# Performance work log

Hardware: AMD Instinct MI355X
Metric: run time of the kernel (lower is better)

The kernel has to match this reference:

```python
import jax, jax.numpy as jnp
import numpy as np
from jax import lax

BIG = jnp.float32(1e10)  # initial 'infinite' min-distance


def farthest_point_sampling(points, nsamples):
    """Exact iterative FPS. points: (B, P, 3) -> indices (B, nsamples) int32.

    The KD-tree partitioning in QuickFPS is an acceleration structure; the
    reference math is the canonical running-min-distance / argmax FPS.
    """
    B, P, _ = points.shape

    def step(carry, _):
        min_d, last_idx = carry
        # (B, 1, 3) coordinates of the most recently selected point
        last_pt = jnp.take_along_axis(points, last_idx[:, None, None], axis=1)
        d = jnp.sum((points - last_pt) ** 2, axis=-1)  # (B, P)
        min_d = jnp.minimum(min_d, d)
        nxt = jnp.argmax(min_d, axis=-1).astype(jnp.int32)  # (B,)
        return (min_d, nxt), nxt

    init_idx = jnp.zeros((B,), jnp.int32)  # CUDA FPS starts from point 0
    init_d = jnp.full((B, P), BIG, dtype=points.dtype)
    (_, _), rest = lax.scan(step, (init_d, init_idx), None, length=nsamples - 1)
    # rest: (nsamples-1, B) -> (B, nsamples)
    indices = jnp.concatenate([init_idx[None, :], rest], axis=0).T
    return indices


def setup_inputs() -> dict:
    key = jax.random.key(0)
    points = jax.random.normal(key, (32, 65536, 3), dtype=jnp.float32)
    return {"points": points}


def reference(points):
    nsamples = 1024
    indices = farthest_point_sampling(points, nsamples)  # (B, nsamples)
    # gather_points: (B, nsamples, 3)
    sampled_points = jnp.take_along_axis(points, indices[:, :, None], axis=1)
    return indices, sampled_points
```

## Files before the change

kernel.cpp:

```cpp
#include <hip/hip_runtime.h>

#define NB 32
#define NP 65536
#define NS 1024
#define NT 1024

typedef unsigned long long u64;
typedef unsigned int u32;

#define BPB 8
#define CHUNK (NP / BPB)
#define PPT2 (CHUNK / NT)

__global__ __launch_bounds__(NT) void fps_slots(const float* __restrict__ pts,
                                                float* __restrict__ out,
                                                u64* __restrict__ slots) {
#pragma clang fp contract(off)
    const int bid = blockIdx.x;
    const int b = bid >> 3;
    const int j = bid & 7;
    const int t = threadIdx.x;
    const int base = j * CHUNK;
    const float* __restrict__ pb = pts + (size_t)b * NP * 3;
    float* __restrict__ out_idx = out + (size_t)b * NS;
    float* __restrict__ out_pts = out + (size_t)NB * NS + (size_t)b * NS * 3;
    u64* __restrict__ slot_b = slots + (size_t)b * NS * BPB;

    __shared__ float P[CHUNK * 3];
    __shared__ u64 cand[NT / 64];
    __shared__ int sel_hist[NS];
    __shared__ float qsh[3];

    {
        const float4* __restrict__ src4 = (const float4*)(pb + (size_t)base * 3);
        float4* dst4 = (float4*)P;
#pragma unroll
        for (int k = 0; k < (CHUNK * 3 / 4) / NT; ++k) dst4[t + k * NT] = src4[t + k * NT];
    }

    float md[PPT2];
#pragma unroll
    for (int i = 0; i < PPT2; ++i) md[i] = 1e10f;

    if (t == 0) {
        sel_hist[0] = 0;
        if (j == 0) out_idx[0] = 0.0f;
        qsh[0] = pb[0]; qsh[1] = pb[1]; qsh[2] = pb[2];
    }
    __syncthreads();

    float qx = qsh[0], qy = qsh[1], qz = qsh[2];

    const int wave = t >> 6;
    const int lane = t & 63;

    for (int s = 1; s < NS; ++s) {
        float bestv = -1.0f;
        int besti = 0;
#pragma unroll
        for (int i = 0; i < PPT2; ++i) {
            const int li = t + i * NT;
            const float* __restrict__ p = P + li * 3;
            float dx = p[0] - qx;
            float dy = p[1] - qy;
            float dz = p[2] - qz;
            float d = (dx * dx + dy * dy) + dz * dz;
            float nmd = fminf(md[i], d);
            md[i] = nmd;
            if (nmd > bestv) { bestv = nmd; besti = li; }
        }
        u64 pk = ((u64)__float_as_uint(bestv) << 32) |
                 (u64)(0xFFFFFFFFu - (u32)(base + besti));
#pragma unroll
        for (int m = 32; m >= 1; m >>= 1) {
            u64 o = __shfl_xor(pk, m, 64);
            pk = (o > pk) ? o : pk;
        }
        if (lane == 0) cand[wave] = pk;
        __syncthreads();
        if (wave == 0) {
            u64 c = (lane < 16) ? cand[lane] : 0ull;
#pragma unroll
            for (int m = 8; m >= 1; m >>= 1) {
                u64 o = __shfl_xor(c, m, 64);
                c = (o > c) ? o : c;
            }
            if (lane == 0) {
                __hip_atomic_store(&slot_b[(size_t)s * BPB + j], c,
                                   __ATOMIC_RELAXED, __HIP_MEMORY_SCOPE_AGENT);
            }
            u64 x = 0;
            if (lane < BPB) {
                const u64* sp = &slot_b[(size_t)s * BPB + lane];
                while ((x = __hip_atomic_load(sp, __ATOMIC_RELAXED,
                                              __HIP_MEMORY_SCOPE_AGENT)) == 0ull) {
                    __builtin_amdgcn_s_sleep(1);
                }
            }
#pragma unroll
            for (int m = 4; m >= 1; m >>= 1) {
                u64 o = __shfl_xor(x, m, 64);
                x = (o > x) ? o : x;
            }
            if (lane == 0) {
                int w = (int)(0xFFFFFFFFu - (u32)(x & 0xFFFFFFFFull));
                sel_hist[s] = w;
                const float* __restrict__ q = pb + (size_t)w * 3;
                qsh[0] = q[0]; qsh[1] = q[1]; qsh[2] = q[2];
                if (j == 0) out_idx[s] = (float)w;
            }
        }
        __syncthreads();
        qx = qsh[0]; qy = qsh[1]; qz = qsh[2];
    }

    if (j == 0) {
        const int gi = sel_hist[t];
        const float* __restrict__ p = pb + (size_t)gi * 3;
        out_pts[(size_t)t * 3 + 0] = p[0];
        out_pts[(size_t)t * 3 + 1] = p[1];
        out_pts[(size_t)t * 3 + 2] = p[2];
    }
}

__global__ __launch_bounds__(NT) void fps_multi(const float* __restrict__ pts,
                                                float* __restrict__ out,
                                                u64* __restrict__ winner,
                                                u32* __restrict__ count) {
#pragma clang fp contract(off)
    const int bid = blockIdx.x;
    const int b = bid >> 3;
    const int j = bid & 7;
    const int t = threadIdx.x;
    const int base = j * CHUNK;
    const float* __restrict__ pb = pts + (size_t)b * NP * 3;
    float* __restrict__ out_idx = out + (size_t)b * NS;
    float* __restrict__ out_pts = out + (size_t)NB * NS + (size_t)b * NS * 3;
    u64* __restrict__ win_b = winner + (size_t)b * NS;
    u32* __restrict__ cnt_b = count + (size_t)b * NS;

    __shared__ float P[CHUNK * 3];
    __shared__ u64 cand[NT / 64];
    __shared__ int sel_hist[NS];
    __shared__ float qsh[3];

    {
        const float4* __restrict__ src4 = (const float4*)(pb + (size_t)base * 3);
        float4* dst4 = (float4*)P;
#pragma unroll
        for (int k = 0; k < (CHUNK * 3 / 4) / NT; ++k) dst4[t + k * NT] = src4[t + k * NT];
    }
    float md[PPT2];
#pragma unroll
    for (int i = 0; i < PPT2; ++i) md[i] = 1e10f;
    if (t == 0) {
        sel_hist[0] = 0;
        if (j == 0) out_idx[0] = 0.0f;
        qsh[0] = pb[0]; qsh[1] = pb[1]; qsh[2] = pb[2];
    }
    __syncthreads();
    float qx = qsh[0], qy = qsh[1], qz = qsh[2];
    const int wave = t >> 6;
    const int lane = t & 63;
    for (int s = 1; s < NS; ++s) {
        float bestv = -1.0f;
        int besti = 0;
#pragma unroll
        for (int i = 0; i < PPT2; ++i) {
            const int li = t + i * NT;
            const float* __restrict__ p = P + li * 3;
            float dx = p[0] - qx, dy = p[1] - qy, dz = p[2] - qz;
            float d = (dx * dx + dy * dy) + dz * dz;
            float nmd = fminf(md[i], d);
            md[i] = nmd;
            if (nmd > bestv) { bestv = nmd; besti = li; }
        }
        u64 pk = ((u64)__float_as_uint(bestv) << 32) |
                 (u64)(0xFFFFFFFFu - (u32)(base + besti));
#pragma unroll
        for (int m = 32; m >= 1; m >>= 1) {
            u64 o = __shfl_xor(pk, m, 64);
            pk = (o > pk) ? o : pk;
        }
        if (lane == 0) cand[wave] = pk;
        __syncthreads();
        if (t == 0) {
            u64 c = cand[0];
#pragma unroll
            for (int w = 1; w < NT / 64; ++w) c = (cand[w] > c) ? cand[w] : c;
            atomicMax(win_b + s, c);
            __threadfence();
            atomicAdd(cnt_b + s, 1u);
            while (__hip_atomic_load(cnt_b + s, __ATOMIC_ACQUIRE,
                                     __HIP_MEMORY_SCOPE_AGENT) < BPB) {
                __builtin_amdgcn_s_sleep(2);
            }
            u64 wv = __hip_atomic_load(win_b + s, __ATOMIC_ACQUIRE,
                                       __HIP_MEMORY_SCOPE_AGENT);
            int w = (int)(0xFFFFFFFFu - (u32)(wv & 0xFFFFFFFFull));
            sel_hist[s] = w;
            const float* __restrict__ q = pb + (size_t)w * 3;
            qsh[0] = q[0]; qsh[1] = q[1]; qsh[2] = q[2];
            if (j == 0) out_idx[s] = (float)w;
        }
        __syncthreads();
        qx = qsh[0]; qy = qsh[1]; qz = qsh[2];
    }
    if (j == 0) {
        const int gi = sel_hist[t];
        const float* __restrict__ p = pb + (size_t)gi * 3;
        out_pts[(size_t)t * 3 + 0] = p[0];
        out_pts[(size_t)t * 3 + 1] = p[1];
        out_pts[(size_t)t * 3 + 2] = p[2];
    }
}

extern "C" void kernel_launch(void* const* d_in, const int* in_sizes, int n_in,
                              void* d_out, int out_size, void* d_ws, size_t ws_size,
                              hipStream_t stream) {
    const float* pts = (const float*)d_in[0];
    float* out = (float*)d_out;
    (void)in_sizes; (void)n_in; (void)out_size;

    const size_t slot_bytes = (size_t)NB * NS * BPB * sizeof(u64);
    const size_t win_bytes = (size_t)NB * NS * sizeof(u64);
    const size_t cnt_bytes = (size_t)NB * NS * sizeof(u32);
    if (ws_size >= slot_bytes) {
        u64* slots = (u64*)d_ws;
        hipMemsetAsync(d_ws, 0, slot_bytes, stream);
        void* args[] = {(void*)&pts, (void*)&out, (void*)&slots};
        hipLaunchCooperativeKernel((const void*)fps_slots, dim3(NB * BPB), dim3(NT),
                                   args, 0, stream);
    } else {
        u64* winner = (u64*)d_ws;
        u32* count = (u32*)((char*)d_ws + win_bytes);
        hipMemsetAsync(d_ws, 0, win_bytes + cnt_bytes, stream);
        void* args[] = {(void*)&pts, (void*)&out, (void*)&winner, (void*)&count};
        hipLaunchCooperativeKernel((const void*)fps_multi, dim3(NB * BPB), dim3(NT),
                                   args, 0, stream);
    }
}
```

Before: 2.616 ms.

## Pad points to float4 in LDS and publish winner coordinates in sync slots

Adds a new primary kernel that stores the point chunk in shared memory padded to float4, so each point is read with one vector LDS load instead of three scalar loads. Each block now publishes its local winner's coordinates alongside its packed key in a 32-byte slot, written with cache-bypassing dwordx4 stores. Readers take the next query point from the winning slot by shuffle, removing the dependent global load of the winner's coordinates from the per-step critical path. The cost is a larger workspace, inline assembly with a torn-read check (matching key halves in both 16-byte parts), and 33% more LDS for the padded layout. The old fps_multi fallback is removed.

New measurement: 2.558 ms. -2.2%, faster.

```diff
diff --git a/kernel.cpp b/kernel.cpp
--- a/kernel.cpp
+++ b/kernel.cpp
@@ -4,13 +4,162 @@
 #define NP 65536
 #define NS 1024
 #define NT 1024
-
-typedef unsigned long long u64;
-typedef unsigned int u32;
-
 #define BPB 8
 #define CHUNK (NP / BPB)
 #define PPT2 (CHUNK / NT)
+
+typedef unsigned long long u64;
+typedef unsigned int u32;
+typedef int int4v __attribute__((ext_vector_type(4)));
+
+__global__ __launch_bounds__(NT) void fps_v6(const float* __restrict__ pts,
+                                             float* __restrict__ out,
+                                             u32* __restrict__ slots) {
+#pragma clang fp contract(off)
+    const int bid = blockIdx.x;
+    const int b = bid >> 3;
+    const int j = bid & 7;
+    const int t = threadIdx.x;
+    const int base = j * CHUNK;
+    const float* __restrict__ pb = pts + (size_t)b * NP * 3;
+    float* __restrict__ out_idx = out + (size_t)b * NS;
+    float* __restrict__ out_pts = out + (size_t)NB * NS + (size_t)b * NS * 3;
+    u32* __restrict__ slot_b = slots + (size_t)b * NS * BPB * 8;
+
+    __shared__ float4 P4[CHUNK];
+    __shared__ u64 cand[NT / 64];
+    __shared__ int sel_hist[NS];
+    __shared__ float qsh[3];
+
+    {
+        const float4* __restrict__ src4 = (const float4*)(pb + (size_t)base * 3);
+#pragma unroll
+        for (int k2 = 0; k2 < CHUNK / 4 / NT; ++k2) {
+            const int g = t + k2 * NT;
+            float4 A = src4[g * 3 + 0];
+            float4 B = src4[g * 3 + 1];
+            float4 C = src4[g * 3 + 2];
+            P4[g * 4 + 0] = make_float4(A.x, A.y, A.z, 0.f);
+            P4[g * 4 + 1] = make_float4(A.w, B.x, B.y, 0.f);
+            P4[g * 4 + 2] = make_float4(B.z, B.w, C.x, 0.f);
+            P4[g * 4 + 3] = make_float4(C.y, C.z, C.w, 0.f);
+        }
+    }
+
+    float md[PPT2];
+#pragma unroll
+    for (int i = 0; i < PPT2; ++i) md[i] = 1e10f;
+
+    if (t == 0) {
+        sel_hist[0] = 0;
+        if (j == 0) out_idx[0] = 0.0f;
+        qsh[0] = pb[0]; qsh[1] = pb[1]; qsh[2] = pb[2];
+    }
+    __syncthreads();
+
+    float qx = qsh[0], qy = qsh[1], qz = qsh[2];
+
+    const int wave = t >> 6;
+    const int lane = t & 63;
+
+    for (int s = 1; s < NS; ++s) {
+        float bestv = -1.0f;
+        int besti = 0;
+#pragma unroll
+        for (int i = 0; i < PPT2; ++i) {
+            const int li = t + i * NT;
+            float4 p = P4[li];
+            float dx = p.x - qx;
+            float dy = p.y - qy;
+            float dz = p.z - qz;
+            float d = (dx * dx + dy * dy) + dz * dz;
+            float nmd = fminf(md[i], d);
+            md[i] = nmd;
+            if (nmd > bestv) { bestv = nmd; besti = li; }
+        }
+        u64 pk = ((u64)__float_as_uint(bestv) << 32) |
+                 (u64)(0xFFFFFFFFu - (u32)(base + besti));
+#pragma unroll
+        for (int m = 32; m >= 1; m >>= 1) {
+            u64 o = __shfl_xor(pk, m, 64);
+            pk = (o > pk) ? o : pk;
+        }
+        if (lane == 0) cand[wave] = pk;
+        __syncthreads();
+        if (wave == 0) {
+            u64 c = (lane < 16) ? cand[lane] : 0ull;
+#pragma unroll
+            for (int m = 8; m >= 1; m >>= 1) {
+                u64 o = __shfl_xor(c, m, 64);
+                c = (o > c) ? o : c;
+            }
+            if (lane == 0) {
+                const int gwin = (int)(0xFFFFFFFFu - (u32)(c & 0xFFFFFFFFull));
+                const int lwin = gwin - base;
+                float4 pw = P4[lwin];
+                int4v h0, h1;
+                h0.x = (int)(u32)(c & 0xFFFFFFFFull);
+                h0.y = (int)(u32)(c >> 32);
+                h0.z = __float_as_int(pw.x);
+                h0.w = __float_as_int(pw.y);
+                h1.x = h0.x;
+                h1.y = h0.y;
+                h1.z = __float_as_int(pw.z);
+                h1.w = 0;
+                u32* sp = slot_b + ((size_t)s * BPB + j) * 8;
+                asm volatile(
+                    "global_store_dwordx4 %0, %2, off sc0 sc1\n\t"
+                    "global_store_dwordx4 %1, %3, off sc0 sc1"
+                    :: "v"(sp), "v"(sp + 4), "v"(h0), "v"(h1) : "memory");
+            }
+            u64 k = 0;
+            float wx = 0.f, wy = 0.f, wz = 0.f;
+            if (lane < BPB) {
+                const u32* pp = slot_b + ((size_t)s * BPB + lane) * 8;
+                int4v a, bb;
+                for (;;) {
+                    asm volatile(
+                        "global_load_dwordx4 %0, %2, off sc0 sc1\n\t"
+                        "global_load_dwordx4 %1, %3, off sc0 sc1\n\t"
+                        "s_waitcnt vmcnt(0)"
+                        : "=&v"(a), "=&v"(bb)
+                        : "v"(pp), "v"(pp + 4) : "memory");
+                    if (a.x != 0 && a.x == bb.x && a.y == bb.y) break;
+                    __builtin_amdgcn_s_sleep(1);
+                }
+                k = ((u64)(u32)a.y << 32) | (u32)a.x;
+                wx = __int_as_float(a.z);
+                wy = __int_as_float(a.w);
+                wz = __int_as_float(bb.z);
+            }
+#pragma unroll
+            for (int m = 4; m >= 1; m >>= 1) {
+                u64 o = __shfl_xor(k, m, 64);
+                k = (o > k) ? o : k;
+            }
+            const int g = (int)(0xFFFFFFFFu - (u32)(k & 0xFFFFFFFFull));
+            const int jw = (g >> 13) & 7;
+            float sx = __shfl(wx, jw, 64);
+            float sy = __shfl(wy, jw, 64);
+            float sz = __shfl(wz, jw, 64);
+            if (lane == 0) {
+                sel_hist[s] = g;
+                qsh[0] = sx; qsh[1] = sy; qsh[2] = sz;
+                if (j == 0) out_idx[s] = (float)g;
+            }
+        }
+        __syncthreads();
+        qx = qsh[0]; qy = qsh[1]; qz = qsh[2];
+    }
+
+    if (j == 0) {
+        const int gi = sel_hist[t];
+        const float* __restrict__ p = pb + (size_t)gi * 3;
+        out_pts[(size_t)t * 3 + 0] = p[0];
+        out_pts[(size_t)t * 3 + 1] = p[1];
+        out_pts[(size_t)t * 3 + 2] = p[2];
+    }
+}
 
 __global__ __launch_bounds__(NT) void fps_slots(const float* __restrict__ pts,
                                                 float* __restrict__ out,
@@ -37,119 +186,6 @@
 #pragma unroll
         for (int k = 0; k < (CHUNK * 3 / 4) / NT; ++k) dst4[t + k * NT] = src4[t + k * NT];
     }
-
-    float md[PPT2];
-#pragma unroll
-    for (int i = 0; i < PPT2; ++i) md[i] = 1e10f;
-
-    if (t == 0) {
-        sel_hist[0] = 0;
-        if (j == 0) out_idx[0] = 0.0f;
-        qsh[0] = pb[0]; qsh[1] = pb[1]; qsh[2] = pb[2];
-    }
-    __syncthreads();
-
-    float qx = qsh[0], qy = qsh[1], qz = qsh[2];
-
-    const int wave = t >> 6;
-    const int lane = t & 63;
-
-    for (int s = 1; s < NS; ++s) {
-        float bestv = -1.0f;
-        int besti = 0;
-#pragma unroll
-        for (int i = 0; i < PPT2; ++i) {
-            const int li = t + i * NT;
-            const float* __restrict__ p = P + li * 3;
-            float dx = p[0] - qx;
-            float dy = p[1] - qy;
-            float dz = p[2] - qz;
-            float d = (dx * dx + dy * dy) + dz * dz;
-            float nmd = fminf(md[i], d);
-            md[i] = nmd;
-            if (nmd > bestv) { bestv = nmd; besti = li; }
-        }
-        u64 pk = ((u64)__float_as_uint(bestv) << 32) |
-                 (u64)(0xFFFFFFFFu - (u32)(base + besti));
-#pragma unroll
-        for (int m = 32; m >= 1; m >>= 1) {
-            u64 o = __shfl_xor(pk, m, 64);
-            pk = (o > pk) ? o : pk;
-        }
-        if (lane == 0) cand[wave] = pk;
-        __syncthreads();
-        if (wave == 0) {
-            u64 c = (lane < 16) ? cand[lane] : 0ull;
-#pragma unroll
-            for (int m = 8; m >= 1; m >>= 1) {
-                u64 o = __shfl_xor(c, m, 64);
-                c = (o > c) ? o : c;
-            }
-            if (lane == 0) {
-                __hip_atomic_store(&slot_b[(size_t)s * BPB + j], c,
-                                   __ATOMIC_RELAXED, __HIP_MEMORY_SCOPE_AGENT);
-            }
-            u64 x = 0;
-            if (lane < BPB) {
-                const u64* sp = &slot_b[(size_t)s * BPB + lane];
-                while ((x = __hip_atomic_load(sp, __ATOMIC_RELAXED,
-                                              __HIP_MEMORY_SCOPE_AGENT)) == 0ull) {
-                    __builtin_amdgcn_s_sleep(1);
-                }
-            }
-#pragma unroll
-            for (int m = 4; m >= 1; m >>= 1) {
-                u64 o = __shfl_xor(x, m, 64);
-                x = (o > x) ? o : x;
-            }
-            if (lane == 0) {
-                int w = (int)(0xFFFFFFFFu - (u32)(x & 0xFFFFFFFFull));
-                sel_hist[s] = w;
-                const float* __restrict__ q = pb + (size_t)w * 3;
-                qsh[0] = q[0]; qsh[1] = q[1]; qsh[2] = q[2];
-                if (j == 0) out_idx[s] = (float)w;
-            }
-        }
-        __syncthreads();
-        qx = qsh[0]; qy = qsh[1]; qz = qsh[2];
-    }
-
-    if (j == 0) {
-        const int gi = sel_hist[t];
-        const float* __restrict__ p = pb + (size_t)gi * 3;
-        out_pts[(size_t)t * 3 + 0] = p[0];
-        out_pts[(size_t)t * 3 + 1] = p[1];
-        out_pts[(size_t)t * 3 + 2] = p[2];
-    }
-}
-
-__global__ __launch_bounds__(NT) void fps_multi(const float* __restrict__ pts,
-                                                float* __restrict__ out,
-                                                u64* __restrict__ winner,
-                                                u32* __restrict__ count) {
-#pragma clang fp contract(off)
-    const int bid = blockIdx.x;
-    const int b = bid >> 3;
-    const int j = bid & 7;
-    const int t = threadIdx.x;
-    const int base = j * CHUNK;
-    const float* __restrict__ pb = pts + (size_t)b * NP * 3;
-    float* __restrict__ out_idx = out + (size_t)b * NS;
-    float* __restrict__ out_pts = out + (size_t)NB * NS + (size_t)b * NS * 3;
-    u64* __restrict__ win_b = winner + (size_t)b * NS;
-    u32* __restrict__ cnt_b = count + (size_t)b * NS;
-
-    __shared__ float P[CHUNK * 3];
-    __shared__ u64 cand[NT / 64];
-    __shared__ int sel_hist[NS];
-    __shared__ float qsh[3];
-
-    {
-        const float4* __restrict__ src4 = (const float4*)(pb + (size_t)base * 3);
-        float4* dst4 = (float4*)P;
-#pragma unroll
-        for (int k = 0; k < (CHUNK * 3 / 4) / NT; ++k) dst4[t + k * NT] = src4[t + k * NT];
-    }
     float md[PPT2];
 #pragma unroll
     for (int i = 0; i < PPT2; ++i) md[i] = 1e10f;
@@ -184,24 +220,37 @@
         }
         if (lane == 0) cand[wave] = pk;
         __syncthreads();
-        if (t == 0) {
-            u64 c = cand[0];
-#pragma unroll
-            for (int w = 1; w < NT / 64; ++w) c = (cand[w] > c) ? cand[w] : c;
-            atomicMax(win_b + s, c);
-            __threadfence();
-            atomicAdd(cnt_b + s, 1u);
-            while (__hip_atomic_load(cnt_b + s, __ATOMIC_ACQUIRE,
-                                     __HIP_MEMORY_SCOPE_AGENT) < BPB) {
-                __builtin_amdgcn_s_sleep(2);
-            }
-            u64 wv = __hip_atomic_load(win_b + s, __ATOMIC_ACQUIRE,
-                                       __HIP_MEMORY_SCOPE_AGENT);
-            int w = (int)(0xFFFFFFFFu - (u32)(wv & 0xFFFFFFFFull));
-            sel_hist[s] = w;
-            const float* __restrict__ q = pb + (size_t)w * 3;
-            qsh[0] = q[0]; qsh[1] = q[1]; qsh[2] = q[2];
-            if (j == 0) out_idx[s] = (float)w;
+        if (wave == 0) {
+            u64 c = (lane < 16) ? cand[lane] : 0ull;
+#pragma unroll
+            for (int m = 8; m >= 1; m >>= 1) {
+                u64 o = __shfl_xor(c, m, 64);
+                c = (o > c) ? o : c;
+            }
+            if (lane == 0) {
+                __hip_atomic_store(&slot_b[(size_t)s * BPB + j], c,
+                                   __ATOMIC_RELAXED, __HIP_MEMORY_SCOPE_AGENT);
+            }
+            u64 x = 0;
+            if (lane < BPB) {
+                const u64* sp = &slot_b[(size_t)s * BPB + lane];
+                while ((x = __hip_atomic_load(sp, __ATOMIC_RELAXED,
+                                              __HIP_MEMORY_SCOPE_AGENT)) == 0ull) {
+                    __builtin_amdgcn_s_sleep(1);
+                }
+            }
+#pragma unroll
+            for (int m = 4; m >= 1; m >>= 1) {
+                u64 o = __shfl_xor(x, m, 64);
+                x = (o > x) ? o : x;
+            }
+            if (lane == 0) {
+                int w = (int)(0xFFFFFFFFu - (u32)(x & 0xFFFFFFFFull));
+                sel_hist[s] = w;
+                const float* __restrict__ q = pb + (size_t)w * 3;
+                qsh[0] = q[0]; qsh[1] = q[1]; qsh[2] = q[2];
+                if (j == 0) out_idx[s] = (float)w;
+            }
         }
         __syncthreads();
         qx = qsh[0]; qy = qsh[1]; qz = qsh[2];
@@ -222,21 +271,19 @@
     float* out = (float*)d_out;
     (void)in_sizes; (void)n_in; (void)out_size;
 
+    const size_t v6_bytes = (size_t)NB * NS * BPB * 32;
     const size_t slot_bytes = (size_t)NB * NS * BPB * sizeof(u64);
-    const size_t win_bytes = (size_t)NB * NS * sizeof(u64);
-    const size_t cnt_bytes = (size_t)NB * NS * sizeof(u32);
-    if (ws_size >= slot_bytes) {
+    if (ws_size >= v6_bytes) {
+        u32* slots = (u32*)d_ws;
+        hipMemsetAsync(d_ws, 0, v6_bytes, stream);
+        void* args[] = {(void*)&pts, (void*)&out, (void*)&slots};
+        hipLaunchCooperativeKernel((const void*)fps_v6, dim3(NB * BPB), dim3(NT),
+                                   args, 0, stream);
+    } else {
         u64* slots = (u64*)d_ws;
         hipMemsetAsync(d_ws, 0, slot_bytes, stream);
         void* args[] = {(void*)&pts, (void*)&out, (void*)&slots};
         hipLaunchCooperativeKernel((const void*)fps_slots, dim3(NB * BPB), dim3(NT),
                                    args, 0, stream);
-    } else {
-        u64* winner = (u64*)d_ws;
-        u32* count = (u32*)((char*)d_ws + win_bytes);
-        hipMemsetAsync(d_ws, 0, win_bytes + cnt_bytes, stream);
-        void* args[] = {(void*)&pts, (void*)&out, (void*)&winner, (void*)&count};
-        hipLaunchCooperativeKernel((const void*)fps_multi, dim3(NB * BPB), dim3(NT),
-                                   args, 0, stream);
     }
 }
```
